# Optimization experiments

Hardware: AMD Instinct MI355X
Metric: run time of the kernel (lower is better)

Reference implementation:

```python
import jax, jax.numpy as jnp
import numpy as np

TEMPERATURE = 0.07


def setup_inputs() -> dict:
    key = jax.random.key(0)
    k1, k2 = jax.random.split(key)
    B, V, D = 4096, 5, 512
    img = jax.random.normal(k1, (B, D), dtype=jnp.float32)
    txt = jax.random.normal(k2, (B, V, D), dtype=jnp.float32)
    # module assumes pre-normalized features
    img = img / jnp.linalg.norm(img, axis=-1, keepdims=True)
    txt = txt / jnp.linalg.norm(txt, axis=-1, keepdims=True)
    return {"image_features": img, "text_features_all": txt}


def reference(image_features, text_features_all):
    B, V, D = text_features_all.shape
    text_flat = text_features_all.reshape(B * V, D)          # (BV, D)
    logits = (image_features @ text_flat.T) / TEMPERATURE    # (B, BV)

    # i2t: per image-row, soft targets = 1/V on its V positive texts
    row_lse = jax.nn.logsumexp(logits, axis=1)               # (B,)
    pos_logits = logits.reshape(B, B, V)[jnp.arange(B), jnp.arange(B)]  # (B, V)
    loss_i2t = jnp.mean(row_lse - jnp.mean(pos_logits, axis=1))

    # t2i: per text-column, cross-entropy over B images, target = col // V
    col_lse = jax.nn.logsumexp(logits, axis=0)               # (BV,)
    img_idx = jnp.arange(B * V) // V
    pos_col = logits[img_idx, jnp.arange(B * V)]             # (BV,)
    loss_t2i = jnp.mean(col_lse - pos_col)

    return (loss_i2t + loss_t2i) * 0.5
```

## Files before the change

### kernel.cpp

```cpp
#include <hip/hip_runtime.h>
#include <stdint.h>

#define B_  4096
#define V_  5
#define D_  512
#define NN_ (B_ * V_)
#define NBLK_ 5120
#define NIMG4_ ((B_ * D_) / 4)

#define C_EXP 20.609929155556620f
#define M_SHIFT (1.0f / 0.07f)
#define SCALE1 0x7f7f7f7f

typedef float floatx4 __attribute__((ext_vector_type(4)));
typedef int   intx4   __attribute__((ext_vector_type(4)));
typedef int   intx8   __attribute__((ext_vector_type(8)));

__device__ __forceinline__ void load_lds16(const void* g, void* l) {
  __builtin_amdgcn_global_load_lds(
      (const __attribute__((address_space(1))) unsigned int*)g,
      (__attribute__((address_space(3))) unsigned int*)l,
      16, 0, 0);
}

__global__ void cvt_kernel(const float* __restrict__ img, const float* __restrict__ txt,
                           uint32_t* __restrict__ out32, float* __restrict__ acc) {
  const int tid0 = blockIdx.x * 256 + threadIdx.x;
  if (tid0 < B_ + NN_) acc[tid0] = 0.0f;
#pragma unroll
  for (int it = 0; it < 4; ++it) {
    const int idx = tid0 + it * (3072 * 256);
    float4 v = (idx < NIMG4_) ? ((const float4*)img)[idx]
                              : ((const float4*)txt)[idx - NIMG4_];
    int w = __builtin_amdgcn_cvt_pk_fp8_f32(v.x, v.y, 0, 0);
    w     = __builtin_amdgcn_cvt_pk_fp8_f32(v.z, v.w, w, 1);
    out32[idx] = (uint32_t)w;
  }
}

__global__ __launch_bounds__(256, 4)
void gemm_kernel(const uint8_t* __restrict__ Ah, const uint8_t* __restrict__ Bh,
                 float* __restrict__ row_sum, float* __restrict__ col_sum,
                 float* __restrict__ posPart) {
  __shared__ __align__(16) uint8_t As[2 * 128 * 64];
  __shared__ __align__(16) uint8_t Bs[2 * 128 * 64];
  const int tid  = threadIdx.x;
  const int lane = tid & 63;
  const int w    = tid >> 6;
  const int wm   = w >> 1, wn = w & 1;
  const int m0   = blockIdx.x * 128;
  const int n0   = blockIdx.y * 128;

  floatx4 acc[4][4] = {};

  const int sc = ((lane & 3) ^ ((lane >> 3) & 3)) * 16;
  const uint8_t* gA = Ah + (size_t)(m0 + w * 32 + (lane >> 2)) * D_ + sc;
  const uint8_t* gB = Bh + (size_t)(n0 + w * 32 + (lane >> 2)) * D_ + sc;
  const int lofs = (w * 32) * 64;

  const int fr  = lane & 15;
  const int swz = (fr >> 1) & 3;
  const int qb  = (lane >> 5) & 1;
  const int qh  = (lane >> 4) & 1;
  const int c0  = ((qh * 2 + 0) ^ swz) * 16;
  const int c1  = ((qh * 2 + 1) ^ swz) * 16;
  const int bufo = qb * 8192;

  #define STAGE(s) do {                                            \
    const int kg = (s) * 128;                                      \
    load_lds16(gA + kg,                As + lofs);                 \
    load_lds16(gA + kg + 16 * D_,      As + lofs + 16 * 64);       \
    load_lds16(gB + kg,                Bs + lofs);                 \
    load_lds16(gB + kg + 16 * D_,      Bs + lofs + 16 * 64);       \
    load_lds16(gA + kg + 64,           As + 8192 + lofs);          \
    load_lds16(gA + kg + 64 + 16 * D_, As + 8192 + lofs + 16 * 64);\
    load_lds16(gB + kg + 64,           Bs + 8192 + lofs);          \
    load_lds16(gB + kg + 64 + 16 * D_, Bs + 8192 + lofs + 16 * 64);\
  } while (0)

  STAGE(0);

#pragma unroll
  for (int ss = 0; ss < 4; ++ss) {
    __syncthreads();

    intx8 af[4], bf[4];
#pragma unroll
    for (int f = 0; f < 4; ++f) {
      const uint8_t* Ar = As + bufo + (wm * 64 + f * 16 + fr) * 64;
      const uint8_t* Br = Bs + bufo + (wn * 64 + f * 16 + fr) * 64;
      intx4 alo = *(const intx4*)(Ar + c0);
      intx4 ahi = *(const intx4*)(Ar + c1);
      intx4 blo = *(const intx4*)(Br + c0);
      intx4 bhi = *(const intx4*)(Br + c1);
      af[f] = __builtin_shufflevector(alo, ahi, 0, 1, 2, 3, 4, 5, 6, 7);
      bf[f] = __builtin_shufflevector(blo, bhi, 0, 1, 2, 3, 4, 5, 6, 7);
    }

    __syncthreads();

    if (ss < 3) STAGE(ss + 1);

#pragma unroll
    for (int mf = 0; mf < 4; ++mf)
#pragma unroll
      for (int nf = 0; nf < 4; ++nf)
        acc[mf][nf] = __builtin_amdgcn_mfma_scale_f32_16x16x128_f8f6f4(
            af[mf], bf[nf], acc[mf][nf],
            0, 0,
            0, SCALE1,
            0, SCALE1);
  }
  #undef STAGE

  {
    float ps = 0.0f;
    const int iLo = n0 / 5, iHi = (n0 + 127) / 5;
    if (iHi >= m0 && iLo < m0 + 128) {
      const int rbase = m0 + wm * 64 + ((lane >> 4) << 2);
#pragma unroll
      for (int nf = 0; nf < 4; ++nf) {
        const int ci = (n0 + wn * 64 + nf * 16 + (lane & 15)) / 5;
#pragma unroll
        for (int mf = 0; mf < 4; ++mf)
#pragma unroll
          for (int r = 0; r < 4; ++r)
            if (rbase + mf * 16 + r == ci) ps += acc[mf][nf][r];
      }
    }
    for (int o = 32; o; o >>= 1) ps += __shfl_xor(ps, o);
    __shared__ float pls[4];
    if (lane == 0) pls[w] = ps;
    __syncthreads();
    if (tid == 0)
      posPart[blockIdx.y * 32 + blockIdx.x] = pls[0] + pls[1] + pls[2] + pls[3];
  }

#pragma unroll
  for (int mf = 0; mf < 4; ++mf)
#pragma unroll
    for (int nf = 0; nf < 4; ++nf)
#pragma unroll
      for (int r = 0; r < 4; ++r)
        acc[mf][nf][r] = exp2f(acc[mf][nf][r] * C_EXP - C_EXP);

  float cs[4];
#pragma unroll
  for (int nf = 0; nf < 4; ++nf) {
    float s = 0.0f;
#pragma unroll
    for (int mf = 0; mf < 4; ++mf)
      s += acc[mf][nf][0] + acc[mf][nf][1] + acc[mf][nf][2] + acc[mf][nf][3];
    s += __shfl_xor(s, 16);
    s += __shfl_xor(s, 32);
    cs[nf] = s;
  }
  {
    int g = lane >> 4;
    float v = (g == 0) ? cs[0] : (g == 1) ? cs[1] : (g == 2) ? cs[2] : cs[3];
    atomicAdd(&col_sum[n0 + wn * 64 + (g << 4) + (lane & 15)], v);
  }

#pragma unroll
  for (int mf = 0; mf < 4; ++mf) {
    floatx4 t = acc[mf][0] + acc[mf][1] + acc[mf][2] + acc[mf][3];
#pragma unroll
    for (int r = 0; r < 4; ++r) {
      float s = t[r];
      s += __shfl_xor(s, 1); s += __shfl_xor(s, 2);
      s += __shfl_xor(s, 4); s += __shfl_xor(s, 8);
      t[r] = s;
    }
    if ((lane & 15) < 4) {
      int q = lane & 3;
      float v = (q == 0) ? t[0] : (q == 1) ? t[1] : (q == 2) ? t[2] : t[3];
      atomicAdd(&row_sum[m0 + wm * 64 + mf * 16 + ((lane >> 4) << 2) + q], v);
    }
  }
}

__global__ void finish_kernel(const float* __restrict__ acc, const float* __restrict__ posPart,
                              float* __restrict__ out) {
  int tid = threadIdx.x;
  float sA = 0.0f, sB = 0.0f, sP = 0.0f;
  for (int i = tid; i < B_;    i += 1024) sA += logf(acc[i]);
  for (int i = tid; i < NN_;   i += 1024) sB += logf(acc[B_ + i]);
  for (int i = tid; i < NBLK_; i += 1024) sP += posPart[i];
  float s = sA * (1.0f / B_) + sB * (1.0f / NN_)
          - sP * (2.0f * M_SHIFT / (float)NN_);
  for (int o = 32; o; o >>= 1) s += __shfl_xor(s, o);
  __shared__ float ls[16];
  int lane = tid & 63, w = tid >> 6;
  if (lane == 0) ls[w] = s;
  __syncthreads();
  if (tid == 0) {
    float tot = 0.0f;
#pragma unroll
    for (int i = 0; i < 16; ++i) tot += ls[i];
    out[0] = M_SHIFT + 0.5f * tot;
  }
}

extern "C" void kernel_launch(void* const* d_in, const int* in_sizes, int n_in,
                              void* d_out, int out_size, void* d_ws, size_t ws_size,
                              hipStream_t stream) {
  const float* img = (const float*)d_in[0];
  const float* txt = (const float*)d_in[1];

  const size_t fp8Bytes = (size_t)(B_ * D_ + NN_ * D_);
  const size_t needBytes = fp8Bytes + (size_t)(B_ + NN_ + NBLK_) * 4;
  if (ws_size < needBytes) return;

  uint8_t* Ah  = (uint8_t*)d_ws;
  uint8_t* Bh  = Ah + (size_t)B_ * D_;
  float* acc   = (float*)((char*)d_ws + fp8Bytes);
  float* row_s = acc;
  float* col_s = acc + B_;
  float* posP  = acc + B_ + NN_;

  cvt_kernel   <<<3072, 256, 0, stream>>>(img, txt, (uint32_t*)Ah, acc);
  gemm_kernel  <<<dim3(32, 160), 256, 0, stream>>>(Ah, Bh, row_s, col_s, posP);
  finish_kernel<<<1, 1024, 0, stream>>>(acc, posP, (float*)d_out);
}
```

Measured before the change: 154.6 us.

## Enlarge GEMM tile to 256x256 with 8 waves and explicit double-buffered pipeline

The fused FP8 GEMM+exp reduction moves from 128x128 tiles with 4 waves to 256x256 tiles with 8 waves, each wave computing 128x64. The K loop now uses 128-byte K steps with two LDS buffers, manual vmcnt waits and raw barriers so loads overlap MFMA work. It also adds a swizzled block order for L2 locality and raises wave priority around the MFMAs. The intent is to cut global/LDS traffic per FLOP and reduce atomics and block count, at the cost of more registers, 128KB of LDS per block and lower occupancy.

```diff
diff --git a/kernel.cpp b/kernel.cpp
--- a/kernel.cpp
+++ b/kernel.cpp
@@ -5,7 +5,7 @@
 #define V_  5
 #define D_  512
 #define NN_ (B_ * V_)
-#define NBLK_ 5120
+#define NBLK_ 1280
 #define NIMG4_ ((B_ * D_) / 4)
 
 #define C_EXP 20.609929155556620f
@@ -38,106 +38,124 @@
   }
 }
 
-__global__ __launch_bounds__(256, 4)
+__global__ __launch_bounds__(512, 2)
 void gemm_kernel(const uint8_t* __restrict__ Ah, const uint8_t* __restrict__ Bh,
                  float* __restrict__ row_sum, float* __restrict__ col_sum,
                  float* __restrict__ posPart) {
-  __shared__ __align__(16) uint8_t As[2 * 128 * 64];
-  __shared__ __align__(16) uint8_t Bs[2 * 128 * 64];
+  __shared__ __align__(16) uint8_t As[2 * 256 * 128];
+  __shared__ __align__(16) uint8_t Bs[2 * 256 * 128];
   const int tid  = threadIdx.x;
   const int lane = tid & 63;
   const int w    = tid >> 6;
-  const int wm   = w >> 1, wn = w & 1;
-  const int m0   = blockIdx.x * 128;
-  const int n0   = blockIdx.y * 128;
-
-  floatx4 acc[4][4] = {};
-
-  const int sc = ((lane & 3) ^ ((lane >> 3) & 3)) * 16;
-  const uint8_t* gA = Ah + (size_t)(m0 + w * 32 + (lane >> 2)) * D_ + sc;
-  const uint8_t* gB = Bh + (size_t)(n0 + w * 32 + (lane >> 2)) * D_ + sc;
-  const int lofs = (w * 32) * 64;
-
-  const int fr  = lane & 15;
-  const int swz = (fr >> 1) & 3;
-  const int qb  = (lane >> 5) & 1;
-  const int qh  = (lane >> 4) & 1;
-  const int c0  = ((qh * 2 + 0) ^ swz) * 16;
-  const int c1  = ((qh * 2 + 1) ^ swz) * 16;
-  const int bufo = qb * 8192;
-
-  #define STAGE(s) do {                                            \
-    const int kg = (s) * 128;                                      \
-    load_lds16(gA + kg,                As + lofs);                 \
-    load_lds16(gA + kg + 16 * D_,      As + lofs + 16 * 64);       \
-    load_lds16(gB + kg,                Bs + lofs);                 \
-    load_lds16(gB + kg + 16 * D_,      Bs + lofs + 16 * 64);       \
-    load_lds16(gA + kg + 64,           As + 8192 + lofs);          \
-    load_lds16(gA + kg + 64 + 16 * D_, As + 8192 + lofs + 16 * 64);\
-    load_lds16(gB + kg + 64,           Bs + 8192 + lofs);          \
-    load_lds16(gB + kg + 64 + 16 * D_, Bs + 8192 + lofs + 16 * 64);\
+  const int wm   = w >> 2;
+  const int wn   = w & 3;
+
+  const int lin = blockIdx.y * 16 + blockIdx.x;
+  const int swz = (lin & 7) * 160 + (lin >> 3);
+  const int m0  = (swz & 15) * 256;
+  const int n0  = (swz >> 4) * 256;
+
+  floatx4 acc[8][4] = {};
+
+  const int srow = lane >> 3;
+  const int soff = ((lane & 7) ^ srow) * 16;
+  const uint8_t* gA = Ah + (size_t)(m0 + w * 32 + srow) * D_ + soff;
+  const uint8_t* gB = Bh + (size_t)(n0 + w * 32 + srow) * D_ + soff;
+  uint8_t* lA = As + w * 4096;
+  uint8_t* lB = Bs + w * 4096;
+
+  #define STAGE(t, buf) do {                                       \
+    const int kk = (t) * 128;                                      \
+    load_lds16(gA + kk,            lA + (buf) * 32768);            \
+    load_lds16(gA + kk +  8 * D_,  lA + (buf) * 32768 + 1024);     \
+    load_lds16(gA + kk + 16 * D_,  lA + (buf) * 32768 + 2048);     \
+    load_lds16(gA + kk + 24 * D_,  lA + (buf) * 32768 + 3072);     \
+    load_lds16(gB + kk,            lB + (buf) * 32768);            \
+    load_lds16(gB + kk +  8 * D_,  lB + (buf) * 32768 + 1024);     \
+    load_lds16(gB + kk + 16 * D_,  lB + (buf) * 32768 + 2048);     \
+    load_lds16(gB + kk + 24 * D_,  lB + (buf) * 32768 + 3072);     \
   } while (0)
 
-  STAGE(0);
-
-#pragma unroll
-  for (int ss = 0; ss < 4; ++ss) {
-    __syncthreads();
-
-    intx8 af[4], bf[4];
-#pragma unroll
-    for (int f = 0; f < 4; ++f) {
-      const uint8_t* Ar = As + bufo + (wm * 64 + f * 16 + fr) * 64;
-      const uint8_t* Br = Bs + bufo + (wn * 64 + f * 16 + fr) * 64;
-      intx4 alo = *(const intx4*)(Ar + c0);
-      intx4 ahi = *(const intx4*)(Ar + c1);
-      intx4 blo = *(const intx4*)(Br + c0);
-      intx4 bhi = *(const intx4*)(Br + c1);
-      af[f] = __builtin_shufflevector(alo, ahi, 0, 1, 2, 3, 4, 5, 6, 7);
-      bf[f] = __builtin_shufflevector(blo, bhi, 0, 1, 2, 3, 4, 5, 6, 7);
-    }
-
-    __syncthreads();
-
-    if (ss < 3) STAGE(ss + 1);
-
-#pragma unroll
-    for (int mf = 0; mf < 4; ++mf)
+  STAGE(0, 0);
+  STAGE(1, 1);
+
+  const int fr = lane & 15;
+  const int q  = lane >> 4;
+  const int cA = ((q * 2) ^ (fr & 7)) * 16;
+
+#pragma unroll
+  for (int t = 0; t < 4; ++t) {
+    if (t < 3) asm volatile("s_waitcnt vmcnt(8)" ::: "memory");
+    else       asm volatile("s_waitcnt vmcnt(0)" ::: "memory");
+    __builtin_amdgcn_s_barrier();
+    __builtin_amdgcn_sched_barrier(0);
+
+    const uint8_t* Ab = As + (t & 1) * 32768 + (wm * 128 + fr) * 128;
+    const uint8_t* Bb = Bs + (t & 1) * 32768 + (wn * 64  + fr) * 128;
+
+    intx8 bf[4];
+#pragma unroll
+    for (int nf = 0; nf < 4; ++nf) {
+      intx4 lo = *(const intx4*)(Bb + nf * 2048 + cA);
+      intx4 hi = *(const intx4*)(Bb + nf * 2048 + (cA ^ 16));
+      bf[nf] = __builtin_shufflevector(lo, hi, 0, 1, 2, 3, 4, 5, 6, 7);
+    }
+
+    __builtin_amdgcn_s_setprio(1);
+#pragma unroll
+    for (int mf = 0; mf < 8; ++mf) {
+      intx4 lo = *(const intx4*)(Ab + mf * 2048 + cA);
+      intx4 hi = *(const intx4*)(Ab + mf * 2048 + (cA ^ 16));
+      intx8 af = __builtin_shufflevector(lo, hi, 0, 1, 2, 3, 4, 5, 6, 7);
 #pragma unroll
       for (int nf = 0; nf < 4; ++nf)
         acc[mf][nf] = __builtin_amdgcn_mfma_scale_f32_16x16x128_f8f6f4(
-            af[mf], bf[nf], acc[mf][nf],
+            af, bf[nf], acc[mf][nf],
             0, 0,
             0, SCALE1,
             0, SCALE1);
+    }
+    __builtin_amdgcn_s_setprio(0);
+
+    if (t < 2) {
+      asm volatile("s_waitcnt lgkmcnt(0)" ::: "memory");
+      __builtin_amdgcn_sched_barrier(0);
+      __builtin_amdgcn_s_barrier();
+      __builtin_amdgcn_sched_barrier(0);
+      STAGE(t + 2, t & 1);
+    }
   }
   #undef STAGE
 
   {
     float ps = 0.0f;
-    const int iLo = n0 / 5, iHi = (n0 + 127) / 5;
-    if (iHi >= m0 && iLo < m0 + 128) {
-      const int rbase = m0 + wm * 64 + ((lane >> 4) << 2);
+    const int iLo = n0 / 5, iHi = (n0 + 255) / 5;
+    if (iHi >= m0 && iLo < m0 + 256) {
+      const int rbase = m0 + wm * 128 + (q << 2);
 #pragma unroll
       for (int nf = 0; nf < 4; ++nf) {
-        const int ci = (n0 + wn * 64 + nf * 16 + (lane & 15)) / 5;
-#pragma unroll
-        for (int mf = 0; mf < 4; ++mf)
+        const int ci = (n0 + wn * 64 + nf * 16 + fr) / 5;
+#pragma unroll
+        for (int mf = 0; mf < 8; ++mf)
 #pragma unroll
           for (int r = 0; r < 4; ++r)
             if (rbase + mf * 16 + r == ci) ps += acc[mf][nf][r];
       }
     }
     for (int o = 32; o; o >>= 1) ps += __shfl_xor(ps, o);
-    __shared__ float pls[4];
+    __shared__ float pls[8];
     if (lane == 0) pls[w] = ps;
     __syncthreads();
-    if (tid == 0)
-      posPart[blockIdx.y * 32 + blockIdx.x] = pls[0] + pls[1] + pls[2] + pls[3];
-  }
-
-#pragma unroll
-  for (int mf = 0; mf < 4; ++mf)
+    if (tid == 0) {
+      float s = 0.0f;
+#pragma unroll
+      for (int i = 0; i < 8; ++i) s += pls[i];
+      posPart[swz] = s;
+    }
+  }
+
+#pragma unroll
+  for (int mf = 0; mf < 8; ++mf)
 #pragma unroll
     for (int nf = 0; nf < 4; ++nf)
 #pragma unroll
@@ -149,20 +167,19 @@
   for (int nf = 0; nf < 4; ++nf) {
     float s = 0.0f;
 #pragma unroll
-    for (int mf = 0; mf < 4; ++mf)
+    for (int mf = 0; mf < 8; ++mf)
       s += acc[mf][nf][0] + acc[mf][nf][1] + acc[mf][nf][2] + acc[mf][nf][3];
     s += __shfl_xor(s, 16);
     s += __shfl_xor(s, 32);
     cs[nf] = s;
   }
   {
-    int g = lane >> 4;
-    float v = (g == 0) ? cs[0] : (g == 1) ? cs[1] : (g == 2) ? cs[2] : cs[3];
-    atomicAdd(&col_sum[n0 + wn * 64 + (g << 4) + (lane & 15)], v);
-  }
-
-#pragma unroll
-  for (int mf = 0; mf < 4; ++mf) {
+    float v = (q == 0) ? cs[0] : (q == 1) ? cs[1] : (q == 2) ? cs[2] : cs[3];
+    atomicAdd(&col_sum[n0 + wn * 64 + (q << 4) + fr], v);
+  }
+
+#pragma unroll
+  for (int mf = 0; mf < 8; ++mf) {
     floatx4 t = acc[mf][0] + acc[mf][1] + acc[mf][2] + acc[mf][3];
 #pragma unroll
     for (int r = 0; r < 4; ++r) {
@@ -172,9 +189,9 @@
       t[r] = s;
     }
     if ((lane & 15) < 4) {
-      int q = lane & 3;
-      float v = (q == 0) ? t[0] : (q == 1) ? t[1] : (q == 2) ? t[2] : t[3];
-      atomicAdd(&row_sum[m0 + wm * 64 + mf * 16 + ((lane >> 4) << 2) + q], v);
+      int rr = lane & 3;
+      float v = (rr == 0) ? t[0] : (rr == 1) ? t[1] : (rr == 2) ? t[2] : t[3];
+      atomicAdd(&row_sum[m0 + wm * 128 + mf * 16 + (q << 2) + rr], v);
     }
   }
 }
@@ -219,6 +236,6 @@
   float* posP  = acc + B_ + NN_;
 
   cvt_kernel   <<<3072, 256, 0, stream>>>(img, txt, (uint32_t*)Ah, acc);
-  gemm_kernel  <<<dim3(32, 160), 256, 0, stream>>>(Ah, Bh, row_s, col_s, posP);
+  gemm_kernel  <<<dim3(16, 80), 512, 0, stream>>>(Ah, Bh, row_s, col_s, posP);
   finish_kernel<<<1, 1024, 0, stream>>>(acc, posP, (float*)d_out);
 }
```

Result: slower. 168.7 us (+9.1%).
